# Performance work log

Hardware: AMD Instinct MI355X
Metric: run time of the kernel (lower is better)

Reference implementation:

```python
import jax, jax.numpy as jnp
import numpy as np

T, N, E, IN, H, H2, H3, B, AF = 12, 50000, 800000, 12, 128, 64, 32, 4096, 10
BN_EPS = 1e-5


def _gin_mlp(h, w1, b1, g, be, rm, rv, w2, b2):
    # Linear -> ReLU -> BatchNorm1d (eval: running stats) -> Dropout(eval=id) -> Linear -> ReLU
    h = jax.nn.relu(h @ w1.T + b1)
    h = (h - rm) * (g * jax.lax.rsqrt(rv + BN_EPS)) + be
    return jax.nn.relu(h @ w2.T + b2)


def _gin_conv(x, edge_src, edge_dst, mlp_params):
    # GINConv with eps=0: MLP(x + sum_{j in N(i)} x_j), scatter-add over edges
    agg = jax.ops.segment_sum(x[edge_src], edge_dst, num_segments=x.shape[0])
    return _gin_mlp(x + agg, *mlp_params)


def _gru(xs, wih, whh, bih, bhh):
    # torch.nn.GRU, 1 layer, h0 = zeros. xs: [T, N, H_in]
    h0 = jnp.zeros((xs.shape[1], whh.shape[1]), xs.dtype)

    def step(h, x):
        gi = x @ wih.T + bih
        gh = h @ whh.T + bhh
        ir, iz, inn = jnp.split(gi, 3, axis=-1)
        hr, hz, hn = jnp.split(gh, 3, axis=-1)
        r = jax.nn.sigmoid(ir + hr)
        z = jax.nn.sigmoid(iz + hz)
        n = jnp.tanh(inn + r * hn)
        h_new = (1.0 - z) * n + z * h
        return h_new, h_new

    h_last, ys = jax.lax.scan(step, h0, xs)
    return ys, h_last


def _forward(floats, edge_src, edge_dst, target_idx):
    (x_seq, apart_feature,
     c1_w1, c1_b1, c1_g, c1_be, c1_rm, c1_rv, c1_w2, c1_b2,
     c2_w1, c2_b1, c2_g, c2_be, c2_rm, c2_rv, c2_w2, c2_b2,
     gru_wih, gru_whh, gru_bih, gru_bhh,
     fc1_w, fc1_b, fc2_w, fc2_b, fc3_w, fc3_b) = floats

    c1 = (c1_w1, c1_b1, c1_g, c1_be, c1_rm, c1_rv, c1_w2, c1_b2)
    c2 = (c2_w1, c2_b1, c2_g, c2_be, c2_rm, c2_rv, c2_w2, c2_b2)

    # conv1 per time slot (lax.map keeps the E x H gather intermediate per-step)
    # extra torch.relu after conv1 is a no-op since the MLP ends in ReLU
    emb = jax.lax.map(lambda xt: _gin_conv(xt, edge_src, edge_dst, c1), x_seq)
    seq, _ = _gru(emb, gru_wih, gru_whh, gru_bih, gru_bhh)
    emb2 = jax.lax.map(lambda xt: _gin_conv(xt, edge_src, edge_dst, c2), seq)
    _, h_last = _gru(emb2, gru_wih, gru_whh, gru_bih, gru_bhh)  # same GRU weights reused

    feat = jnp.concatenate([h_last[target_idx], apart_feature], axis=1)
    h = jax.nn.leaky_relu(feat @ fc1_w.T + fc1_b, negative_slope=0.1)
    h = jax.nn.leaky_relu(h @ fc2_w.T + fc2_b, negative_slope=0.05)
    return h @ fc3_w.T + fc3_b  # [B, 1]


def setup_inputs() -> dict:
    key = jax.random.key(0)
    ks = jax.random.split(key, 24)
    f32 = jnp.float32
    w = lambda i, shape, fan: jax.random.normal(ks[i], shape, f32) * (1.0 / np.sqrt(fan))
    return {
        "x_seq": jax.random.normal(ks[0], (T, N, IN), f32),
        "apart_feature": jax.random.normal(ks[1], (B, AF), f32),
        "edge_src": jax.random.randint(ks[2], (E,), 0, N, jnp.int32),
        "edge_dst": jax.random.randint(ks[3], (E,), 0, N, jnp.int32),
        "target_idx": jax.random.randint(ks[4], (B,), 0, N, jnp.int32),
        # conv1 MLP
        "c1_w1": w(5, (H, IN), IN), "c1_b1": jnp.zeros((H,), f32),
        "c1_g": jnp.ones((H,), f32), "c1_be": jnp.zeros((H,), f32),
        "c1_rm": jnp.zeros((H,), f32), "c1_rv": jnp.ones((H,), f32),
        "c1_w2": w(6, (H, H), H), "c1_b2": jnp.zeros((H,), f32),
        # conv2 MLP
        "c2_w1": w(7, (H, H), H), "c2_b1": jnp.zeros((H,), f32),
        "c2_g": jnp.ones((H,), f32), "c2_be": jnp.zeros((H,), f32),
        "c2_rm": jnp.zeros((H,), f32), "c2_rv": jnp.ones((H,), f32),
        "c2_w2": w(8, (H, H), H), "c2_b2": jnp.zeros((H,), f32),
        # shared GRU
        "gru_wih": w(9, (3 * H, H), H), "gru_whh": w(10, (3 * H, H), H),
        "gru_bih": jnp.zeros((3 * H,), f32), "gru_bhh": jnp.zeros((3 * H,), f32),
        # head
        "fc1_w": w(11, (H2, H + AF), H + AF), "fc1_b": jnp.zeros((H2,), f32),
        "fc2_w": w(12, (H3, H2), H2), "fc2_b": jnp.zeros((H3,), f32),
        "fc3_w": w(13, (1, H3), H3), "fc3_b": jnp.zeros((1,), f32),
    }


def reference(x_seq, apart_feature,
              c1_w1, c1_b1, c1_g, c1_be, c1_rm, c1_rv, c1_w2, c1_b2,
              c2_w1, c2_b1, c2_g, c2_be, c2_rm, c2_rv, c2_w2, c2_b2,
              gru_wih, gru_whh, gru_bih, gru_bhh,
              fc1_w, fc1_b, fc2_w, fc2_b, fc3_w, fc3_b,
              edge_src, edge_dst, target_idx):
    floats = (x_seq, apart_feature,
              c1_w1, c1_b1, c1_g, c1_be, c1_rm, c1_rv, c1_w2, c1_b2,
              c2_w1, c2_b1, c2_g, c2_be, c2_rm, c2_rv, c2_w2, c2_b2,
              gru_wih, gru_whh, gru_bih, gru_bhh,
              fc1_w, fc1_b, fc2_w, fc2_b, fc3_w, fc3_b)
    return _forward(floats, edge_src, edge_dst, target_idx)
```

## Files before the change

kernel.cpp:

```cpp
#include <hip/hip_runtime.h>

#define T_STEPS 12
#define NN      50000
#define EE      800000
#define IN_F    12
#define TF12    (T_STEPS * IN_F)
#define HID     128
#define G3      384
#define BB      4096
#define AF_     10
#define BN_EPS  1e-5f
#define LPAD    136
#define NBLK    ((NN + 63) / 64)

typedef unsigned short ushort_t;
typedef __attribute__((ext_vector_type(8))) short bf16x8;
typedef __attribute__((ext_vector_type(4))) float f32x4;

#define MFMA(a, b, c) __builtin_amdgcn_mfma_f32_16x16x32_bf16((a), (b), (c), 0, 0, 0)
#define L2E 1.4426950408889634f

__device__ inline float b2f(ushort_t u) { return __uint_as_float(((unsigned)u) << 16); }
__device__ inline float b2f_lo(unsigned u) { return __uint_as_float(u << 16); }
__device__ inline float b2f_hi(unsigned u) { return __uint_as_float(u & 0xffff0000u); }
__device__ inline ushort_t f2b(float f) {
    unsigned u = __float_as_uint(f);
    return (ushort_t)((u + 0x7fffu + ((u >> 16) & 1u)) >> 16);
}
__device__ inline float sigm(float x) {
    return __builtin_amdgcn_rcpf(1.f + __builtin_amdgcn_exp2f(-x * L2E));
}
__device__ inline float ftanh(float x) {
    float xx = fminf(fmaxf(x, -15.f), 15.f);
    float t = __builtin_amdgcn_exp2f(2.f * L2E * xx);
    return (t - 1.f) * __builtin_amdgcn_rcpf(t + 1.f);
}

#define ALIGN_UP(x) (((x) + 255) & ~(size_t)255)
#define SZ_DEG    ALIGN_UP((size_t)NN * 4)
#define SZ_RP     ALIGN_UP((size_t)(NN + 1) * 4)
#define SZ_CUR    ALIGN_UP((size_t)NN * 4)
#define SZ_COL    ALIGN_UP((size_t)EE * 4)
#define SZ_XT     ALIGN_UP((size_t)NN * TF12 * 4)
#define SZ_EMB    ALIGN_UP((size_t)T_STEPS * NN * HID * 2)
#define SZ_NHB    ALIGN_UP((size_t)NN * HID * 2)
#define SZ_W128   ALIGN_UP((size_t)HID * HID * 2)
#define SZ_WGRU   ALIGN_UP((size_t)G3 * HID * 2)
#define WS_NEED   (SZ_DEG + SZ_RP + SZ_CUR + SZ_COL + 2 * SZ_XT + SZ_EMB + 3 * SZ_NHB + 3 * SZ_W128 + 2 * SZ_WGRU)

__device__ __align__(256) char g_static_pool[WS_NEED];

__global__ void zero_out_kernel(float* out, int n) {
    int i = blockIdx.x * blockDim.x + threadIdx.x;
    if (i < n) out[i] = 0.f;
}

__global__ void cvt5_kernel(const float* s0, ushort_t* d0, int n0,
                            const float* s1, ushort_t* d1, int n1,
                            const float* s2, ushort_t* d2, int n2,
                            const float* s3, ushort_t* d3, int n3,
                            const float* s4, ushort_t* d4, int n4) {
    int i = blockIdx.x * blockDim.x + threadIdx.x;
    if (i < n0) d0[i] = f2b(s0[i]);
    i -= n0;
    if (i >= 0 && i < n1) d1[i] = f2b(s1[i]);
    i -= n1;
    if (i >= 0 && i < n2) d2[i] = f2b(s2[i]);
    i -= n2;
    if (i >= 0 && i < n3) d3[i] = f2b(s3[i]);
    i -= n3;
    if (i >= 0 && i < n4) d4[i] = f2b(s4[i]);
}

__global__ void init_kernel(int* deg, ushort_t* h1, ushort_t* h2) {
    int i = blockIdx.x * blockDim.x + threadIdx.x;
    if (i < NN) deg[i] = 0;
    if (i < NN * HID) { h1[i] = 0; h2[i] = 0; }
}

__global__ void hist_kernel(const int* __restrict__ dst, int* __restrict__ deg, int E) {
    int e = blockIdx.x * blockDim.x + threadIdx.x;
    if (e < E) {
        unsigned d = (unsigned)dst[e];
        if (d < NN) atomicAdd(&deg[d], 1);
    }
}

__global__ __launch_bounds__(1024) void scan_kernel(const int* __restrict__ deg,
                                                    int* __restrict__ row_ptr,
                                                    int* __restrict__ cursor, int n) {
    __shared__ int wsum[16];
    __shared__ int carry_s;
    int tid = threadIdx.x;
    int wid = tid >> 6, lane = tid & 63;
    if (tid == 0) { carry_s = 0; row_ptr[0] = 0; }
    __syncthreads();
    for (int base = 0; base < n; base += 1024) {
        int i = base + tid;
        int v = (i < n) ? deg[i] : 0;
        int x = v;
#pragma unroll
        for (int off = 1; off < 64; off <<= 1) {
            int t = __shfl_up(x, (unsigned)off);
            if (lane >= off) x += t;
        }
        if (lane == 63) wsum[wid] = x;
        __syncthreads();
        if (tid == 0) {
            int a = 0;
#pragma unroll
            for (int w = 0; w < 16; ++w) { int t = wsum[w]; wsum[w] = a; a += t; }
        }
        __syncthreads();
        int incl = carry_s + wsum[wid] + x;
        if (i < n) {
            row_ptr[i + 1] = incl;
            cursor[i] = incl - v;
        }
        __syncthreads();
        if (tid == 1023) carry_s = incl;
        __syncthreads();
    }
}

__global__ void scatter_kernel(const int* __restrict__ src, const int* __restrict__ dst,
                               int* __restrict__ cursor, int* __restrict__ col, int E) {
    int e = blockIdx.x * blockDim.x + threadIdx.x;
    if (e < E) {
        unsigned d = (unsigned)dst[e];
        if (d < NN) {
            int pos = atomicAdd(&cursor[d], 1);
            if ((unsigned)pos < (unsigned)EE) col[pos] = src[e];
        }
    }
}

__global__ void transpose_x_kernel(const float* __restrict__ x_seq, float* __restrict__ xT) {
    int g = blockIdx.x * blockDim.x + threadIdx.x;
    if (g >= NN * TF12) return;
    int n = g / TF12;
    int u = g - n * TF12;
    int t = u / IN_F;
    int f = u - t * IN_F;
    xT[g] = x_seq[(size_t)t * NN * IN_F + (size_t)n * IN_F + f];
}

__global__ __launch_bounds__(512) void agg12t_kernel(const float* __restrict__ xT,
                                                     const int* __restrict__ rp,
                                                     const int* __restrict__ col,
                                                     float* __restrict__ xagg, int E) {
    int node = blockIdx.x * 8 + (threadIdx.x >> 6);
    int lane = threadIdx.x & 63;
    if (node >= NN) return;
    const float2* pself = (const float2*)(xT + (size_t)node * TF12);
    float2 a = pself[lane];
    float a2 = (lane < 16) ? xT[(size_t)node * TF12 + 128 + lane] : 0.f;
    int e0 = rp[node], e1 = rp[node + 1];
    if (e1 > E) e1 = E;
    int e = e0;
    for (; e + 1 < e1; e += 2) {
        unsigned c0 = (unsigned)col[e], c1 = (unsigned)col[e + 1];
        c0 = (c0 < NN) ? c0 : 0; c1 = (c1 < NN) ? c1 : 0;
        const float2* p0 = (const float2*)(xT + (size_t)c0 * TF12);
        const float2* p1 = (const float2*)(xT + (size_t)c1 * TF12);
        float2 v0 = p0[lane];
        float2 v1 = p1[lane];
        a.x += v0.x + v1.x;
        a.y += v0.y + v1.y;
        if (lane < 16)
            a2 += xT[(size_t)c0 * TF12 + 128 + lane] + xT[(size_t)c1 * TF12 + 128 + lane];
    }
    for (; e < e1; ++e) {
        unsigned c = (unsigned)col[e];
        if (c < NN) {
            const float2* pn = (const float2*)(xT + (size_t)c * TF12);
            float2 v = pn[lane];
            a.x += v.x;
            a.y += v.y;
            if (lane < 16) a2 += xT[(size_t)c * TF12 + 128 + lane];
        }
    }
    ((float2*)(xagg + (size_t)node * TF12))[lane] = a;
    if (lane < 16) xagg[(size_t)node * TF12 + 128 + lane] = a2;
}

__global__ __launch_bounds__(512) void conv1c_all_kernel(const float* __restrict__ xagg,
                                                         ushort_t* __restrict__ emb,
                                                         const float* __restrict__ W1, const float* __restrict__ b1,
                                                         const float* __restrict__ gg, const float* __restrict__ be,
                                                         const float* __restrict__ rm, const float* __restrict__ rv,
                                                         const ushort_t* __restrict__ w2b, const float* __restrict__ b2) {
    __shared__ float xs[64][IN_F + 1];
    __shared__ ushort_t l1[64][LPAD];
    int t = blockIdx.y;
    ushort_t* et = emb + (size_t)t * NN * HID;
    int tid = threadIdx.x;
    int r0 = blockIdx.x * 64;
    for (int u = tid; u < 64 * IN_F; u += 512) {
        int r = u / IN_F, f = u - r * IN_F;
        int row = r0 + r;
        xs[r][f] = (row < NN) ? xagg[(size_t)row * TF12 + t * IN_F + f] : 0.f;
    }
    __syncthreads();
    {
        int j = tid & 127, rb = tid >> 7;
        float sc = gg[j] * rsqrtf(rv[j] + BN_EPS);
        float sh = be[j] - rm[j] * sc;
        float bj = b1[j];
        float wreg[IN_F];
#pragma unroll
        for (int k = 0; k < IN_F; ++k) wreg[k] = W1[j * IN_F + k];
#pragma unroll
        for (int q = 0; q < 16; ++q) {
            int r = rb + q * 4;
            float s = bj;
#pragma unroll
            for (int k = 0; k < IN_F; ++k) s += xs[r][k] * wreg[k];
            s = fmaxf(s, 0.f);
            l1[r][j] = f2b(s * sc + sh);
        }
    }
    __syncthreads();
    {
        int wave = tid >> 6, lane = tid & 63, li = lane & 15, ks = lane >> 4;
        int jc = wave * 16 + li;
        const ushort_t* pw = w2b + (size_t)jc * HID + ks * 8;
        f32x4 A0 = {0,0,0,0}, A1 = {0,0,0,0}, A2 = {0,0,0,0}, A3 = {0,0,0,0};
#pragma unroll
        for (int k0 = 0; k0 < HID; k0 += 32) {
            bf16x8 wf = *(const bf16x8*)(pw + k0);
            bf16x8 a0 = *(const bf16x8*)&l1[li][ks * 8 + k0];
            bf16x8 a1 = *(const bf16x8*)&l1[li + 16][ks * 8 + k0];
            bf16x8 a2 = *(const bf16x8*)&l1[li + 32][ks * 8 + k0];
            bf16x8 a3 = *(const bf16x8*)&l1[li + 48][ks * 8 + k0];
            A0 = MFMA(a0, wf, A0); A1 = MFMA(a1, wf, A1);
            A2 = MFMA(a2, wf, A2); A3 = MFMA(a3, wf, A3);
        }
        float bj = b2[jc];
#pragma unroll
        for (int q = 0; q < 4; ++q) {
            int rA = r0 + ks * 4 + q, rB = rA + 16, rC = rA + 32, rD = rA + 48;
            if (rA < NN) et[(size_t)rA * HID + jc] = f2b(fmaxf(A0[q] + bj, 0.f));
            if (rB < NN) et[(size_t)rB * HID + jc] = f2b(fmaxf(A1[q] + bj, 0.f));
            if (rC < NN) et[(size_t)rC * HID + jc] = f2b(fmaxf(A2[q] + bj, 0.f));
            if (rD < NN) et[(size_t)rD * HID + jc] = f2b(fmaxf(A3[q] + bj, 0.f));
        }
    }
}

__device__ __forceinline__ void gru_body(const ushort_t* __restrict__ x,
                                         ushort_t* __restrict__ h,
                                         const ushort_t* __restrict__ wih,
                                         const ushort_t* __restrict__ whh,
                                         const float* __restrict__ bih,
                                         const float* __restrict__ bhh, int blk) {
    int tid = threadIdx.x;
    int wave = tid >> 6, lane = tid & 63, li = lane & 15, ks = lane >> 4;
    int r0 = blk * 64;
    int jc = wave * 16 + li;
    const ushort_t* px[4];
    const ushort_t* ph[4];
#pragma unroll
    for (int tt = 0; tt < 4; ++tt) {
        int ra = min(r0 + tt * 16 + li, NN - 1);
        px[tt] = x + (size_t)ra * HID + ks * 8;
        ph[tt] = h + (size_t)ra * HID + ks * 8;
    }
    const ushort_t* pwr = wih + (size_t)jc * HID + ks * 8;
    const ushort_t* pwz = wih + (size_t)(HID + jc) * HID + ks * 8;
    const ushort_t* pwn = wih + (size_t)(2 * HID + jc) * HID + ks * 8;
    const ushort_t* pvr = whh + (size_t)jc * HID + ks * 8;
    const ushort_t* pvz = whh + (size_t)(HID + jc) * HID + ks * 8;
    const ushort_t* pvn = whh + (size_t)(2 * HID + jc) * HID + ks * 8;
    f32x4 Ir[4], Iz[4], In[4], Hr[4], Hz[4], Hn[4];
#pragma unroll
    for (int tt = 0; tt < 4; ++tt) {
        Ir[tt] = (f32x4){0,0,0,0}; Iz[tt] = (f32x4){0,0,0,0}; In[tt] = (f32x4){0,0,0,0};
        Hr[tt] = (f32x4){0,0,0,0}; Hz[tt] = (f32x4){0,0,0,0}; Hn[tt] = (f32x4){0,0,0,0};
    }
#pragma unroll
    for (int k0 = 0; k0 < HID; k0 += 32) {
        bf16x8 wr = *(const bf16x8*)(pwr + k0);
        bf16x8 wz = *(const bf16x8*)(pwz + k0);
        bf16x8 wn = *(const bf16x8*)(pwn + k0);
        bf16x8 vr = *(const bf16x8*)(pvr + k0);
        bf16x8 vz = *(const bf16x8*)(pvz + k0);
        bf16x8 vn = *(const bf16x8*)(pvn + k0);
#pragma unroll
        for (int tt = 0; tt < 4; ++tt) {
            bf16x8 xf = *(const bf16x8*)(px[tt] + k0);
            bf16x8 hf = *(const bf16x8*)(ph[tt] + k0);
            Ir[tt] = MFMA(xf, wr, Ir[tt]);
            Iz[tt] = MFMA(xf, wz, Iz[tt]);
            In[tt] = MFMA(xf, wn, In[tt]);
            Hr[tt] = MFMA(hf, vr, Hr[tt]);
            Hz[tt] = MFMA(hf, vz, Hz[tt]);
            Hn[tt] = MFMA(hf, vn, Hn[tt]);
        }
    }
    float bi_r = bih[jc], bi_z = bih[HID + jc], bi_n = bih[2 * HID + jc];
    float bh_r = bhh[jc], bh_z = bhh[HID + jc], bh_n = bhh[2 * HID + jc];
    float hold[4][4];
#pragma unroll
    for (int tt = 0; tt < 4; ++tt)
#pragma unroll
        for (int q = 0; q < 4; ++q) {
            int rr = min(r0 + tt * 16 + ks * 4 + q, NN - 1);
            hold[tt][q] = b2f(h[(size_t)rr * HID + jc]);
        }
    __syncthreads();
#pragma unroll
    for (int tt = 0; tt < 4; ++tt)
#pragma unroll
        for (int q = 0; q < 4; ++q) {
            int row = r0 + tt * 16 + ks * 4 + q;
            float rg = sigm(Ir[tt][q] + bi_r + Hr[tt][q] + bh_r);
            float zg = sigm(Iz[tt][q] + bi_z + Hz[tt][q] + bh_z);
            float ng = ftanh(In[tt][q] + bi_n + rg * (Hn[tt][q] + bh_n));
            float hv = (1.f - zg) * ng + zg * hold[tt][q];
            if (row < NN) h[(size_t)row * HID + jc] = f2b(hv);
        }
}

__device__ __forceinline__ void mega2_body(const ushort_t* __restrict__ xin2,
                                           ushort_t* __restrict__ h2,
                                           const ushort_t* __restrict__ w1b, const float* __restrict__ b1,
                                           const float* __restrict__ gg, const float* __restrict__ be,
                                           const float* __restrict__ rm, const float* __restrict__ rv,
                                           const ushort_t* __restrict__ w2b, const float* __restrict__ b2,
                                           const ushort_t* __restrict__ wih, const ushort_t* __restrict__ whh,
                                           const float* __restrict__ bih, const float* __restrict__ bhh, int blk) {
    __shared__ ushort_t bufA[64][LPAD];
    __shared__ ushort_t bufB[64][LPAD];
    int tid = threadIdx.x;
    int wave = tid >> 6, lane = tid & 63, li = lane & 15, ks = lane >> 4;
    int r0 = blk * 64;
    int jc = wave * 16 + li;
    f32x4 Hr[4], Hz[4], Hn[4], C1[4];
#pragma unroll
    for (int tt = 0; tt < 4; ++tt) {
        Hr[tt] = (f32x4){0,0,0,0}; Hz[tt] = (f32x4){0,0,0,0};
        Hn[tt] = (f32x4){0,0,0,0}; C1[tt] = (f32x4){0,0,0,0};
    }
    {
        const ushort_t* pw1 = w1b + (size_t)jc * HID + ks * 8;
        const ushort_t* pvr = whh + (size_t)jc * HID + ks * 8;
        const ushort_t* pvz = whh + (size_t)(HID + jc) * HID + ks * 8;
        const ushort_t* pvn = whh + (size_t)(2 * HID + jc) * HID + ks * 8;
        const ushort_t* pa[4];
        const ushort_t* ph[4];
#pragma unroll
        for (int tt = 0; tt < 4; ++tt) {
            int ra = min(r0 + tt * 16 + li, NN - 1);
            pa[tt] = xin2 + (size_t)ra * HID + ks * 8;
            ph[tt] = h2 + (size_t)ra * HID + ks * 8;
        }
#pragma unroll
        for (int k0 = 0; k0 < HID; k0 += 32) {
            bf16x8 w1f = *(const bf16x8*)(pw1 + k0);
            bf16x8 vr = *(const bf16x8*)(pvr + k0);
            bf16x8 vz = *(const bf16x8*)(pvz + k0);
            bf16x8 vn = *(const bf16x8*)(pvn + k0);
#pragma unroll
            for (int tt = 0; tt < 4; ++tt) {
                bf16x8 af = *(const bf16x8*)(pa[tt] + k0);
                bf16x8 hf = *(const bf16x8*)(ph[tt] + k0);
                C1[tt] = MFMA(af, w1f, C1[tt]);
                Hr[tt] = MFMA(hf, vr, Hr[tt]);
                Hz[tt] = MFMA(hf, vz, Hz[tt]);
                Hn[tt] = MFMA(hf, vn, Hn[tt]);
            }
        }
    }
    float hold[4][4];
#pragma unroll
    for (int tt = 0; tt < 4; ++tt)
#pragma unroll
        for (int q = 0; q < 4; ++q) {
            int rr = min(r0 + tt * 16 + ks * 4 + q, NN - 1);
            hold[tt][q] = b2f(h2[(size_t)rr * HID + jc]);
        }
    {
        float sc = gg[jc] * rsqrtf(rv[jc] + BN_EPS);
        float sh = be[jc] - rm[jc] * sc;
        float bj = b1[jc];
#pragma unroll
        for (int tt = 0; tt < 4; ++tt)
#pragma unroll
            for (int q = 0; q < 4; ++q)
                bufB[tt * 16 + ks * 4 + q][jc] = f2b(fmaxf(C1[tt][q] + bj, 0.f) * sc + sh);
    }
    __syncthreads();
    {
        const ushort_t* pw2 = w2b + (size_t)jc * HID + ks * 8;
        f32x4 C2[4];
#pragma unroll
        for (int tt = 0; tt < 4; ++tt) C2[tt] = (f32x4){0,0,0,0};
#pragma unroll
        for (int k0 = 0; k0 < HID; k0 += 32) {
            bf16x8 wf = *(const bf16x8*)(pw2 + k0);
#pragma unroll
            for (int tt = 0; tt < 4; ++tt) {
                bf16x8 af = *(const bf16x8*)&bufB[li + 16 * tt][ks * 8 + k0];
                C2[tt] = MFMA(af, wf, C2[tt]);
            }
        }
        float bj = b2[jc];
#pragma unroll
        for (int tt = 0; tt < 4; ++tt)
#pragma unroll
            for (int q = 0; q < 4; ++q)
                bufA[tt * 16 + ks * 4 + q][jc] = f2b(fmaxf(C2[tt][q] + bj, 0.f));
    }
    __syncthreads();
    {
        const ushort_t* pwr = wih + (size_t)jc * HID + ks * 8;
        const ushort_t* pwz = wih + (size_t)(HID + jc) * HID + ks * 8;
        const ushort_t* pwn = wih + (size_t)(2 * HID + jc) * HID + ks * 8;
        f32x4 Ir[4], Iz[4], In[4];
#pragma unroll
        for (int tt = 0; tt < 4; ++tt) {
            Ir[tt] = (f32x4){0,0,0,0}; Iz[tt] = (f32x4){0,0,0,0}; In[tt] = (f32x4){0,0,0,0};
        }
#pragma unroll
        for (int k0 = 0; k0 < HID; k0 += 32) {
            bf16x8 wr = *(const bf16x8*)(pwr + k0);
            bf16x8 wz = *(const bf16x8*)(pwz + k0);
            bf16x8 wn = *(const bf16x8*)(pwn + k0);
#pragma unroll
            for (int tt = 0; tt < 4; ++tt) {
                bf16x8 xf = *(const bf16x8*)&bufA[li + 16 * tt][ks * 8 + k0];
                Ir[tt] = MFMA(xf, wr, Ir[tt]);
                Iz[tt] = MFMA(xf, wz, Iz[tt]);
                In[tt] = MFMA(xf, wn, In[tt]);
            }
        }
        float bi_r = bih[jc], bi_z = bih[HID + jc], bi_n = bih[2 * HID + jc];
        float bh_r = bhh[jc], bh_z = bhh[HID + jc], bh_n = bhh[2 * HID + jc];
#pragma unroll
        for (int tt = 0; tt < 4; ++tt)
#pragma unroll
            for (int q = 0; q < 4; ++q) {
                int row = r0 + tt * 16 + ks * 4 + q;
                float rg = sigm(Ir[tt][q] + bi_r + Hr[tt][q] + bh_r);
                float zg = sigm(Iz[tt][q] + bi_z + Hz[tt][q] + bh_z);
                float ng = ftanh(In[tt][q] + bi_n + rg * (Hn[tt][q] + bh_n));
                float hv = (1.f - zg) * ng + zg * hold[tt][q];
                if (row < NN) h2[(size_t)row * HID + jc] = f2b(hv);
            }
    }
}

__global__ __launch_bounds__(512) void gru_step_kernel(const ushort_t* __restrict__ x, ushort_t* __restrict__ h,
                                                       const ushort_t* __restrict__ wih, const ushort_t* __restrict__ whh,
                                                       const float* __restrict__ bih, const float* __restrict__ bhh) {
    gru_body(x, h, wih, whh, bih, bhh, blockIdx.x);
}

__global__ __launch_bounds__(512) void mega2_kernel(const ushort_t* __restrict__ xin2, ushort_t* __restrict__ h2,
                                                    const ushort_t* __restrict__ w1b, const float* __restrict__ b1,
                                                    const float* __restrict__ gg, const float* __restrict__ be,
                                                    const float* __restrict__ rm, const float* __restrict__ rv,
                                                    const ushort_t* __restrict__ w2b, const float* __restrict__ b2,
                                                    const ushort_t* __restrict__ wih, const ushort_t* __restrict__ whh,
                                                    const float* __restrict__ bih, const float* __restrict__ bhh) {
    mega2_body(xin2, h2, w1b, b1, gg, be, rm, rv, w2b, b2, wih, whh, bih, bhh, blockIdx.x);
}

__global__ __launch_bounds__(512) void fused_mg_kernel(const ushort_t* __restrict__ xin2, ushort_t* __restrict__ h2,
                                                       const ushort_t* __restrict__ w1b, const float* __restrict__ b1,
                                                       const float* __restrict__ gg, const float* __restrict__ be,
                                                       const float* __restrict__ rm, const float* __restrict__ rv,
                                                       const ushort_t* __restrict__ w2b, const float* __restrict__ b2,
                                                       const ushort_t* __restrict__ wih, const ushort_t* __restrict__ whh,
                                                       const float* __restrict__ bih, const float* __restrict__ bhh,
                                                       const ushort_t* __restrict__ emb_next, ushort_t* __restrict__ h1) {
    int b = blockIdx.x;
    if (b < NBLK) {
        mega2_body(xin2, h2, w1b, b1, gg, be, rm, rv, w2b, b2, wih, whh, bih, bhh, b);
    } else {
        gru_body(emb_next, h1, wih, whh, bih, bhh, b - NBLK);
    }
}

__global__ __launch_bounds__(256) void agg128b_kernel(const ushort_t* __restrict__ x,
                                                      const int* __restrict__ rp,
                                                      const int* __restrict__ col,
                                                      ushort_t* __restrict__ out, int E) {
    int node = (blockIdx.x * 256 + threadIdx.x) >> 6;
    int lane = threadIdx.x & 63;
    if (node >= NN) return;
    unsigned v = *(const unsigned*)(x + (size_t)node * HID + lane * 2);
    float s0 = b2f_lo(v);
    float s1 = b2f_hi(v);
    int e0 = rp[node], e1 = rp[node + 1];
    if (e1 > E) e1 = E;
    int e = e0;
    for (; e + 3 < e1; e += 4) {
        unsigned c0 = (unsigned)col[e], c1 = (unsigned)col[e + 1];
        unsigned c2 = (unsigned)col[e + 2], c3 = (unsigned)col[e + 3];
        c0 = (c0 < NN) ? c0 : 0; c1 = (c1 < NN) ? c1 : 0;
        c2 = (c2 < NN) ? c2 : 0; c3 = (c3 < NN) ? c3 : 0;
        unsigned u0 = *(const unsigned*)(x + (size_t)c0 * HID + lane * 2);
        unsigned u1 = *(const unsigned*)(x + (size_t)c1 * HID + lane * 2);
        unsigned u2 = *(const unsigned*)(x + (size_t)c2 * HID + lane * 2);
        unsigned u3 = *(const unsigned*)(x + (size_t)c3 * HID + lane * 2);
        s0 += b2f_lo(u0) + b2f_lo(u1) + b2f_lo(u2) + b2f_lo(u3);
        s1 += b2f_hi(u0) + b2f_hi(u1) + b2f_hi(u2) + b2f_hi(u3);
    }
    for (; e < e1; ++e) {
        unsigned c = (unsigned)col[e];
        if (c < NN) {
            unsigned u = *(const unsigned*)(x + (size_t)c * HID + lane * 2);
            s0 += b2f_lo(u);
            s1 += b2f_hi(u);
        }
    }
    unsigned o = (unsigned)f2b(s0) | ((unsigned)f2b(s1) << 16);
    *(unsigned*)(out + (size_t)node * HID + lane * 2) = o;
}

__global__ __launch_bounds__(64) void head_kernel(const ushort_t* __restrict__ h2, const int* __restrict__ tidx,
                                                  const float* __restrict__ apart,
                                                  const float* __restrict__ w1, const float* __restrict__ b1,
                                                  const float* __restrict__ w2, const float* __restrict__ b2,
                                                  const float* __restrict__ w3, const float* __restrict__ b3,
                                                  float* __restrict__ out) {
    __shared__ float feat[HID + AF_];
    __shared__ float o1[64];
    __shared__ float o2[32];
    int b = blockIdx.x;
    int t = threadIdx.x;
    unsigned node = (unsigned)tidx[b];
    if (node >= NN) node = 0;
    for (int k = t; k < HID; k += 64) feat[k] = b2f(h2[(size_t)node * HID + k]);
    if (t < AF_) feat[HID + t] = apart[(size_t)b * AF_ + t];
    __syncthreads();
    {
        float s = b1[t];
        for (int k = 0; k < HID + AF_; ++k) s += feat[k] * w1[t * (HID + AF_) + k];
        o1[t] = (s > 0.f) ? s : 0.1f * s;
    }
    __syncthreads();
    if (t < 32) {
        float s = b2[t];
        for (int k = 0; k < 64; ++k) s += o1[k] * w2[t * 64 + k];
        o2[t] = (s > 0.f) ? s : 0.05f * s;
    }
    __syncthreads();
    if (t == 0) {
        float s = b3[0];
        for (int k = 0; k < 32; ++k) s += o2[k] * w3[k];
        out[b] = s;
    }
}

extern "C" void kernel_launch(void* const* d_in, const int* in_sizes, int n_in,
                              void* d_out, int out_size, void* d_ws, size_t ws_size,
                              hipStream_t stream) {
    int ie_src = -1, ie_dst = -1, ie_tidx = -1, iw0 = -1;
    bool ok = false;
    if (n_in >= 31 && in_sizes[0] == T_STEPS * NN * IN_F && in_sizes[1] == BB * AF_) {
        if (in_sizes[2] > 100000 && in_sizes[3] == in_sizes[2] && in_sizes[4] == BB &&
            in_sizes[5] == HID * IN_F && in_sizes[11] == HID * HID &&
            in_sizes[21] == G3 * HID && in_sizes[22] == G3 * HID &&
            in_sizes[25] == 64 * (HID + AF_)) {
            ie_src = 2; ie_dst = 3; ie_tidx = 4; iw0 = 5; ok = true;
        } else if (in_sizes[2] == HID * IN_F && in_sizes[8] == HID * HID &&
                   in_sizes[18] == G3 * HID && in_sizes[19] == G3 * HID &&
                   in_sizes[22] == 64 * (HID + AF_) &&
                   in_sizes[28] > 100000 && in_sizes[29] == in_sizes[28] && in_sizes[30] == BB) {
            iw0 = 2; ie_src = 28; ie_dst = 29; ie_tidx = 30; ok = true;
        }
    }
    if (!ok) {
        zero_out_kernel<<<(out_size + 255) / 256, 256, 0, stream>>>((float*)d_out, out_size);
        return;
    }

    const float* x_seq  = (const float*)d_in[0];
    const float* apart  = (const float*)d_in[1];
    const int*   e_src  = (const int*)d_in[ie_src];
    const int*   e_dst  = (const int*)d_in[ie_dst];
    const int*   t_idx  = (const int*)d_in[ie_tidx];
    const float* c1_w1 = (const float*)d_in[iw0 + 0];
    const float* c1_b1 = (const float*)d_in[iw0 + 1];
    const float* c1_g  = (const float*)d_in[iw0 + 2];
    const float* c1_be = (const float*)d_in[iw0 + 3];
    const float* c1_rm = (const float*)d_in[iw0 + 4];
    const float* c1_rv = (const float*)d_in[iw0 + 5];
    const float* c1_w2 = (const float*)d_in[iw0 + 6];
    const float* c1_b2 = (const float*)d_in[iw0 + 7];
    const float* c2_w1 = (const float*)d_in[iw0 + 8];
    const float* c2_b1 = (const float*)d_in[iw0 + 9];
    const float* c2_g  = (const float*)d_in[iw0 + 10];
    const float* c2_be = (const float*)d_in[iw0 + 11];
    const float* c2_rm = (const float*)d_in[iw0 + 12];
    const float* c2_rv = (const float*)d_in[iw0 + 13];
    const float* c2_w2 = (const float*)d_in[iw0 + 14];
    const float* c2_b2 = (const float*)d_in[iw0 + 15];
    const float* g_wih = (const float*)d_in[iw0 + 16];
    const float* g_whh = (const float*)d_in[iw0 + 17];
    const float* g_bih = (const float*)d_in[iw0 + 18];
    const float* g_bhh = (const float*)d_in[iw0 + 19];
    const float* f1_w  = (const float*)d_in[iw0 + 20];
    const float* f1_b  = (const float*)d_in[iw0 + 21];
    const float* f2_w  = (const float*)d_in[iw0 + 22];
    const float* f2_b  = (const float*)d_in[iw0 + 23];
    const float* f3_w  = (const float*)d_in[iw0 + 24];
    const float* f3_b  = (const float*)d_in[iw0 + 25];

    int E = in_sizes[ie_src];
    if (E > EE) E = EE;

    char* base;
    if (ws_size >= WS_NEED) {
        base = (char*)d_ws;
    } else {
        void* sp = nullptr;
        hipGetSymbolAddress(&sp, HIP_SYMBOL(g_static_pool));
        if (sp == nullptr) {
            zero_out_kernel<<<(out_size + 255) / 256, 256, 0, stream>>>((float*)d_out, out_size);
            return;
        }
        base = (char*)sp;
    }
    size_t off = 0;
    auto nxt = [&](size_t bytes) { char* p = base + off; off += bytes; return p; };
    int*      deg      = (int*)nxt(SZ_DEG);
    int*      row_ptr  = (int*)nxt(SZ_RP);
    int*      cursor   = (int*)nxt(SZ_CUR);
    int*      col      = (int*)nxt(SZ_COL);
    float*    xT       = (float*)nxt(SZ_XT);
    float*    xagg     = (float*)nxt(SZ_XT);
    ushort_t* emb      = (ushort_t*)nxt(SZ_EMB);
    ushort_t* xin2     = (ushort_t*)nxt(SZ_NHB);
    ushort_t* h1       = (ushort_t*)nxt(SZ_NHB);
    ushort_t* h2       = (ushort_t*)nxt(SZ_NHB);
    ushort_t* wb_c1w2  = (ushort_t*)nxt(SZ_W128);
    ushort_t* wb_c2w1  = (ushort_t*)nxt(SZ_W128);
    ushort_t* wb_c2w2  = (ushort_t*)nxt(SZ_W128);
    ushort_t* wb_wih   = (ushort_t*)nxt(SZ_WGRU);
    ushort_t* wb_whh   = (ushort_t*)nxt(SZ_WGRU);

    const int NW = 3 * HID * HID + 2 * G3 * HID;
    cvt5_kernel<<<(NW + 255) / 256, 256, 0, stream>>>(c1_w2, wb_c1w2, HID * HID,
                                                      c2_w1, wb_c2w1, HID * HID,
                                                      c2_w2, wb_c2w2, HID * HID,
                                                      g_wih, wb_wih, G3 * HID,
                                                      g_whh, wb_whh, G3 * HID);

    init_kernel<<<(NN * HID + 255) / 256, 256, 0, stream>>>(deg, h1, h2);

    hist_kernel<<<(E + 255) / 256, 256, 0, stream>>>(e_dst, deg, E);
    scan_kernel<<<1, 1024, 0, stream>>>(deg, row_ptr, cursor, NN);
    scatter_kernel<<<(E + 255) / 256, 256, 0, stream>>>(e_src, e_dst, cursor, col, E);

    transpose_x_kernel<<<(NN * TF12 + 255) / 256, 256, 0, stream>>>(x_seq, xT);
    agg12t_kernel<<<(NN + 7) / 8, 512, 0, stream>>>(xT, row_ptr, col, xagg, E);
    conv1c_all_kernel<<<dim3(NBLK, T_STEPS), 512, 0, stream>>>(xagg, emb,
                                                               c1_w1, c1_b1, c1_g, c1_be, c1_rm, c1_rv,
                                                               wb_c1w2, c1_b2);

    gru_step_kernel<<<NBLK, 512, 0, stream>>>(emb, h1, wb_wih, wb_whh, g_bih, g_bhh);
    agg128b_kernel<<<(NN * 64 + 255) / 256, 256, 0, stream>>>(h1, row_ptr, col, xin2, E);
    for (int t = 0; t < T_STEPS - 1; ++t) {
        fused_mg_kernel<<<2 * NBLK, 512, 0, stream>>>(xin2, h2,
                                                      wb_c2w1, c2_b1, c2_g, c2_be, c2_rm, c2_rv,
                                                      wb_c2w2, c2_b2,
                                                      wb_wih, wb_whh, g_bih, g_bhh,
                                                      emb + (size_t)(t + 1) * NN * HID, h1);
        agg128b_kernel<<<(NN * 64 + 255) / 256, 256, 0, stream>>>(h1, row_ptr, col, xin2, E);
    }
    mega2_kernel<<<NBLK, 512, 0, stream>>>(xin2, h2,
                                           wb_c2w1, c2_b1, c2_g, c2_be, c2_rm, c2_rv,
                                           wb_c2w2, c2_b2,
                                           wb_wih, wb_whh, g_bih, g_bhh);

    head_kernel<<<BB, 64, 0, stream>>>(h2, t_idx, apart, f1_w, f1_b, f2_w, f2_b, f3_w, f3_b, (float*)d_out);
}
```

Measured before the change: 2.270 ms.

## Software-pipeline GRU1, aggregation and conv2 stages into one launch per step

Double-buffers the first GRU hidden state and the aggregated conv2 input so that, in each launch, conv2+GRU2 for step m, GRU1 for step m+2 and the neighbour aggregation for step m+1 can run side by side as separate block ranges. This removes the separate agg128b launch per time step and the serialization between aggregation and the fused kernel, cutting launch count and letting the different workloads overlap on the GPU. It costs two extra N×H bf16 buffers and makes the step kernel larger, which may affect register allocation or occupancy. The in-place GRU update and its __syncthreads are removed because the hidden state now reads from one buffer and writes to another.

```diff
diff --git a/kernel.cpp b/kernel.cpp
--- a/kernel.cpp
+++ b/kernel.cpp
@@ -12,6 +12,7 @@
 #define BN_EPS  1e-5f
 #define LPAD    136
 #define NBLK    ((NN + 63) / 64)
+#define AGGB    ((NN + 7) / 8)
 
 typedef unsigned short ushort_t;
 typedef __attribute__((ext_vector_type(8))) short bf16x8;
@@ -46,7 +47,7 @@
 #define SZ_NHB    ALIGN_UP((size_t)NN * HID * 2)
 #define SZ_W128   ALIGN_UP((size_t)HID * HID * 2)
 #define SZ_WGRU   ALIGN_UP((size_t)G3 * HID * 2)
-#define WS_NEED   (SZ_DEG + SZ_RP + SZ_CUR + SZ_COL + 2 * SZ_XT + SZ_EMB + 3 * SZ_NHB + 3 * SZ_W128 + 2 * SZ_WGRU)
+#define WS_NEED   (SZ_DEG + SZ_RP + SZ_CUR + SZ_COL + 2 * SZ_XT + SZ_EMB + 5 * SZ_NHB + 3 * SZ_W128 + 2 * SZ_WGRU)
 
 __device__ __align__(256) char g_static_pool[WS_NEED];
 
@@ -72,10 +73,10 @@
     if (i >= 0 && i < n4) d4[i] = f2b(s4[i]);
 }
 
-__global__ void init_kernel(int* deg, ushort_t* h1, ushort_t* h2) {
+__global__ void init_kernel(int* deg, ushort_t* h1b, ushort_t* h2) {
     int i = blockIdx.x * blockDim.x + threadIdx.x;
     if (i < NN) deg[i] = 0;
-    if (i < NN * HID) { h1[i] = 0; h2[i] = 0; }
+    if (i < NN * HID) { h1b[i] = 0; h2[i] = 0; }
 }
 
 __global__ void hist_kernel(const int* __restrict__ dst, int* __restrict__ deg, int E) {
@@ -249,7 +250,8 @@
 }
 
 __device__ __forceinline__ void gru_body(const ushort_t* __restrict__ x,
-                                         ushort_t* __restrict__ h,
+                                         const ushort_t* __restrict__ hprev,
+                                         ushort_t* __restrict__ hcur,
                                          const ushort_t* __restrict__ wih,
                                          const ushort_t* __restrict__ whh,
                                          const float* __restrict__ bih,
@@ -264,7 +266,7 @@
     for (int tt = 0; tt < 4; ++tt) {
         int ra = min(r0 + tt * 16 + li, NN - 1);
         px[tt] = x + (size_t)ra * HID + ks * 8;
-        ph[tt] = h + (size_t)ra * HID + ks * 8;
+        ph[tt] = hprev + (size_t)ra * HID + ks * 8;
     }
     const ushort_t* pwr = wih + (size_t)jc * HID + ks * 8;
     const ushort_t* pwz = wih + (size_t)(HID + jc) * HID + ks * 8;
@@ -300,25 +302,18 @@
     }
     float bi_r = bih[jc], bi_z = bih[HID + jc], bi_n = bih[2 * HID + jc];
     float bh_r = bhh[jc], bh_z = bhh[HID + jc], bh_n = bhh[2 * HID + jc];
-    float hold[4][4];
-#pragma unroll
-    for (int tt = 0; tt < 4; ++tt)
-#pragma unroll
-        for (int q = 0; q < 4; ++q) {
-            int rr = min(r0 + tt * 16 + ks * 4 + q, NN - 1);
-            hold[tt][q] = b2f(h[(size_t)rr * HID + jc]);
-        }
-    __syncthreads();
 #pragma unroll
     for (int tt = 0; tt < 4; ++tt)
 #pragma unroll
         for (int q = 0; q < 4; ++q) {
             int row = r0 + tt * 16 + ks * 4 + q;
+            int rr = min(row, NN - 1);
+            float hold = b2f(hprev[(size_t)rr * HID + jc]);
             float rg = sigm(Ir[tt][q] + bi_r + Hr[tt][q] + bh_r);
             float zg = sigm(Iz[tt][q] + bi_z + Hz[tt][q] + bh_z);
             float ng = ftanh(In[tt][q] + bi_n + rg * (Hn[tt][q] + bh_n));
-            float hv = (1.f - zg) * ng + zg * hold[tt][q];
-            if (row < NN) h[(size_t)row * HID + jc] = f2b(hv);
+            float hv = (1.f - zg) * ng + zg * hold;
+            if (row < NN) hcur[(size_t)row * HID + jc] = f2b(hv);
         }
 }
 
@@ -451,43 +446,11 @@
     }
 }
 
-__global__ __launch_bounds__(512) void gru_step_kernel(const ushort_t* __restrict__ x, ushort_t* __restrict__ h,
-                                                       const ushort_t* __restrict__ wih, const ushort_t* __restrict__ whh,
-                                                       const float* __restrict__ bih, const float* __restrict__ bhh) {
-    gru_body(x, h, wih, whh, bih, bhh, blockIdx.x);
-}
-
-__global__ __launch_bounds__(512) void mega2_kernel(const ushort_t* __restrict__ xin2, ushort_t* __restrict__ h2,
-                                                    const ushort_t* __restrict__ w1b, const float* __restrict__ b1,
-                                                    const float* __restrict__ gg, const float* __restrict__ be,
-                                                    const float* __restrict__ rm, const float* __restrict__ rv,
-                                                    const ushort_t* __restrict__ w2b, const float* __restrict__ b2,
-                                                    const ushort_t* __restrict__ wih, const ushort_t* __restrict__ whh,
-                                                    const float* __restrict__ bih, const float* __restrict__ bhh) {
-    mega2_body(xin2, h2, w1b, b1, gg, be, rm, rv, w2b, b2, wih, whh, bih, bhh, blockIdx.x);
-}
-
-__global__ __launch_bounds__(512) void fused_mg_kernel(const ushort_t* __restrict__ xin2, ushort_t* __restrict__ h2,
-                                                       const ushort_t* __restrict__ w1b, const float* __restrict__ b1,
-                                                       const float* __restrict__ gg, const float* __restrict__ be,
-                                                       const float* __restrict__ rm, const float* __restrict__ rv,
-                                                       const ushort_t* __restrict__ w2b, const float* __restrict__ b2,
-                                                       const ushort_t* __restrict__ wih, const ushort_t* __restrict__ whh,
-                                                       const float* __restrict__ bih, const float* __restrict__ bhh,
-                                                       const ushort_t* __restrict__ emb_next, ushort_t* __restrict__ h1) {
-    int b = blockIdx.x;
-    if (b < NBLK) {
-        mega2_body(xin2, h2, w1b, b1, gg, be, rm, rv, w2b, b2, wih, whh, bih, bhh, b);
-    } else {
-        gru_body(emb_next, h1, wih, whh, bih, bhh, b - NBLK);
-    }
-}
-
-__global__ __launch_bounds__(256) void agg128b_kernel(const ushort_t* __restrict__ x,
-                                                      const int* __restrict__ rp,
-                                                      const int* __restrict__ col,
-                                                      ushort_t* __restrict__ out, int E) {
-    int node = (blockIdx.x * 256 + threadIdx.x) >> 6;
+__device__ __forceinline__ void agg128b_body(const ushort_t* __restrict__ x,
+                                             const int* __restrict__ rp,
+                                             const int* __restrict__ col,
+                                             ushort_t* __restrict__ out, int E, int blk) {
+    int node = blk * 8 + (threadIdx.x >> 6);
     int lane = threadIdx.x & 63;
     if (node >= NN) return;
     unsigned v = *(const unsigned*)(x + (size_t)node * HID + lane * 2);
@@ -518,6 +481,37 @@
     }
     unsigned o = (unsigned)f2b(s0) | ((unsigned)f2b(s1) << 16);
     *(unsigned*)(out + (size_t)node * HID + lane * 2) = o;
+}
+
+__global__ __launch_bounds__(512) void step_kernel(
+        int has_m, const ushort_t* __restrict__ xm, ushort_t* __restrict__ h2,
+        const ushort_t* __restrict__ w1b, const float* __restrict__ b1,
+        const float* __restrict__ gg, const float* __restrict__ be,
+        const float* __restrict__ rm, const float* __restrict__ rv,
+        const ushort_t* __restrict__ w2b, const float* __restrict__ b2,
+        const ushort_t* __restrict__ wih, const ushort_t* __restrict__ whh,
+        const float* __restrict__ bih, const float* __restrict__ bhh,
+        int has_g, const ushort_t* __restrict__ emb_g,
+        const ushort_t* __restrict__ hprev, ushort_t* __restrict__ hcur,
+        int has_a, const ushort_t* __restrict__ ha, ushort_t* __restrict__ xa,
+        const int* __restrict__ rp, const int* __restrict__ col, int E) {
+    int b = blockIdx.x;
+    if (has_m) {
+        if (b < NBLK) {
+            mega2_body(xm, h2, w1b, b1, gg, be, rm, rv, w2b, b2, wih, whh, bih, bhh, b);
+            return;
+        }
+        b -= NBLK;
+    }
+    if (has_g) {
+        if (b < NBLK) {
+            gru_body(emb_g, hprev, hcur, wih, whh, bih, bhh, b);
+            return;
+        }
+        b -= NBLK;
+    }
+    if (has_a && b < AGGB)
+        agg128b_body(ha, rp, col, xa, E, b);
 }
 
 __global__ __launch_bounds__(64) void head_kernel(const ushort_t* __restrict__ h2, const int* __restrict__ tidx,
@@ -634,8 +628,10 @@
     float*    xT       = (float*)nxt(SZ_XT);
     float*    xagg     = (float*)nxt(SZ_XT);
     ushort_t* emb      = (ushort_t*)nxt(SZ_EMB);
-    ushort_t* xin2     = (ushort_t*)nxt(SZ_NHB);
-    ushort_t* h1       = (ushort_t*)nxt(SZ_NHB);
+    ushort_t* X0       = (ushort_t*)nxt(SZ_NHB);
+    ushort_t* X1       = (ushort_t*)nxt(SZ_NHB);
+    ushort_t* h1a      = (ushort_t*)nxt(SZ_NHB);
+    ushort_t* h1b      = (ushort_t*)nxt(SZ_NHB);
     ushort_t* h2       = (ushort_t*)nxt(SZ_NHB);
     ushort_t* wb_c1w2  = (ushort_t*)nxt(SZ_W128);
     ushort_t* wb_c2w1  = (ushort_t*)nxt(SZ_W128);
@@ -650,7 +646,7 @@
                                                       g_wih, wb_wih, G3 * HID,
                                                       g_whh, wb_whh, G3 * HID);
 
-    init_kernel<<<(NN * HID + 255) / 256, 256, 0, stream>>>(deg, h1, h2);
+    init_kernel<<<(NN * HID + 255) / 256, 256, 0, stream>>>(deg, h1b, h2);
 
     hist_kernel<<<(E + 255) / 256, 256, 0, stream>>>(e_dst, deg, E);
     scan_kernel<<<1, 1024, 0, stream>>>(deg, row_ptr, cursor, NN);
@@ -662,20 +658,37 @@
                                                                c1_w1, c1_b1, c1_g, c1_be, c1_rm, c1_rv,
                                                                wb_c1w2, c1_b2);
 
-    gru_step_kernel<<<NBLK, 512, 0, stream>>>(emb, h1, wb_wih, wb_whh, g_bih, g_bhh);
-    agg128b_kernel<<<(NN * 64 + 255) / 256, 256, 0, stream>>>(h1, row_ptr, col, xin2, E);
-    for (int t = 0; t < T_STEPS - 1; ++t) {
-        fused_mg_kernel<<<2 * NBLK, 512, 0, stream>>>(xin2, h2,
-                                                      wb_c2w1, c2_b1, c2_g, c2_be, c2_rm, c2_rv,
-                                                      wb_c2w2, c2_b2,
-                                                      wb_wih, wb_whh, g_bih, g_bhh,
-                                                      emb + (size_t)(t + 1) * NN * HID, h1);
-        agg128b_kernel<<<(NN * 64 + 255) / 256, 256, 0, stream>>>(h1, row_ptr, col, xin2, E);
-    }
-    mega2_kernel<<<NBLK, 512, 0, stream>>>(xin2, h2,
-                                           wb_c2w1, c2_b1, c2_g, c2_be, c2_rm, c2_rv,
-                                           wb_c2w2, c2_b2,
-                                           wb_wih, wb_whh, g_bih, g_bhh);
+    auto h1buf = [&](int t) { return (t & 1) ? h1b : h1a; };
+    auto xbuf  = [&](int t) { return (t & 1) ? X1 : X0; };
+
+    step_kernel<<<NBLK, 512, 0, stream>>>(0, nullptr, h2,
+                                          wb_c2w1, c2_b1, c2_g, c2_be, c2_rm, c2_rv, wb_c2w2, c2_b2,
+                                          wb_wih, wb_whh, g_bih, g_bhh,
+                                          1, emb, h1b, h1a,
+                                          0, nullptr, nullptr, row_ptr, col, E);
+    step_kernel<<<NBLK + AGGB, 512, 0, stream>>>(0, nullptr, h2,
+                                                 wb_c2w1, c2_b1, c2_g, c2_be, c2_rm, c2_rv, wb_c2w2, c2_b2,
+                                                 wb_wih, wb_whh, g_bih, g_bhh,
+                                                 1, emb + (size_t)1 * NN * HID, h1a, h1b,
+                                                 1, h1a, X0, row_ptr, col, E);
+    for (int m = 0; m <= T_STEPS - 2; ++m) {
+        int g = m + 2;
+        int a = m + 1;
+        int has_g = (g <= T_STEPS - 1) ? 1 : 0;
+        int grid = NBLK + (has_g ? NBLK : 0) + AGGB;
+        step_kernel<<<grid, 512, 0, stream>>>(1, xbuf(m), h2,
+                                              wb_c2w1, c2_b1, c2_g, c2_be, c2_rm, c2_rv, wb_c2w2, c2_b2,
+                                              wb_wih, wb_whh, g_bih, g_bhh,
+                                              has_g,
+                                              emb + (size_t)(has_g ? g : 0) * NN * HID,
+                                              h1buf(g - 1), h1buf(g),
+                                              1, h1buf(a), xbuf(a), row_ptr, col, E);
+    }
+    step_kernel<<<NBLK, 512, 0, stream>>>(1, xbuf(T_STEPS - 1), h2,
+                                          wb_c2w1, c2_b1, c2_g, c2_be, c2_rm, c2_rv, wb_c2w2, c2_b2,
+                                          wb_wih, wb_whh, g_bih, g_bhh,
+                                          0, nullptr, nullptr, nullptr,
+                                          0, nullptr, nullptr, row_ptr, col, E);
 
     head_kernel<<<BB, 64, 0, stream>>>(h2, t_idx, apart, f1_w, f1_b, f2_w, f2_b, f3_w, f3_b, (float*)d_out);
 }
```

Result: slower. 3.106 ms (+36.8%).
